# Optimization experiments

Hardware: AMD Instinct MI355X
Metric: run time of the kernel (lower is better)

## Reference

```python
import jax, jax.numpy as jnp
import numpy as np

TEMPERATURE = 0.07
EPS = 1e-12  # matches torch F.normalize default


def _l2_normalize(x):
    # torch F.normalize: x / max(||x||_2, eps)
    norm = jnp.sqrt(jnp.sum(x * x, axis=-1, keepdims=True))
    return x / jnp.maximum(norm, EPS)


def setup_inputs() -> dict:
    key = jax.random.key(0)
    k1, k2, k3 = jax.random.split(key, 3)
    B, N, D = 4096, 127, 256
    anchor = jax.random.normal(k1, (B, D), dtype=jnp.float32)
    positive = jax.random.normal(k2, (B, D), dtype=jnp.float32)
    negatives = jax.random.normal(k3, (B, N, D), dtype=jnp.float32)
    return {"anchor": anchor, "positive": positive, "negatives": negatives}


def reference(anchor, positive, negatives):
    a = _l2_normalize(anchor)          # [B, D]
    p = _l2_normalize(positive)        # [B, D]
    n = _l2_normalize(negatives)       # [B, N, D]
    pos_scores = jnp.sum(a * p, axis=-1, keepdims=True)   # [B, 1]
    neg_scores = jnp.einsum("bd,bnd->bn", a, n)           # [B, N]
    logits = jnp.concatenate([pos_scores, neg_scores], axis=1) / TEMPERATURE
    # cross-entropy with label 0 for every row
    loss = jnp.mean(jax.nn.logsumexp(logits, axis=-1) - logits[:, 0])
    return loss
```

## Files before the change

### kernel.cpp

```cpp
#include <hip/hip_runtime.h>
#include <math.h>


namespace {
constexpr int B = 4096;
constexpr int N = 127;
constexpr int D = 256;
constexpr int V = N + 1;
constexpr float INV_TEMP = 1.0f / 0.07f;
constexpr float EPS = 1e-12f;

typedef float f32x4 __attribute__((ext_vector_type(4)));

__device__ __forceinline__ float group16_reduce_sum(float v) {
    #pragma unroll
    for (int off = 1; off < 16; off <<= 1) v += __shfl_xor(v, off, 64);
    return v;
}
__device__ __forceinline__ float wave_reduce_sum(float v) {
    #pragma unroll
    for (int off = 32; off > 0; off >>= 1) v += __shfl_xor(v, off, 64);
    return v;
}
__device__ __forceinline__ float wave_reduce_max(float v) {
    #pragma unroll
    for (int off = 32; off > 0; off >>= 1) v = fmaxf(v, __shfl_xor(v, off, 64));
    return v;
}

__device__ __forceinline__ void load4(f32x4 (&buf)[4], const float* p) {
    #pragma unroll
    for (int i = 0; i < 4; ++i)
        buf[i] = *reinterpret_cast<const f32x4*>(p + i * 64);
}

__device__ __forceinline__ void acc4(float& d, float& s,
                                     const f32x4 (&aa)[4], const f32x4 (&x)[4]) {
    float dd = 0.f, ss = 0.f;
    #pragma unroll
    for (int i = 0; i < 4; ++i) {
        dd += aa[i].x * x[i].x + aa[i].y * x[i].y + aa[i].z * x[i].z + aa[i].w * x[i].w;
        ss += x[i].x * x[i].x + x[i].y * x[i].y + x[i].z * x[i].z + x[i].w * x[i].w;
    }
    d = dd; s = ss;
}
}

__global__ __launch_bounds__(256) void infonce_rows(
    const float* __restrict__ anchor,
    const float* __restrict__ positive,
    const float* __restrict__ negatives,
    float* __restrict__ row_loss)
{
    const int b   = blockIdx.x;
    const int tid = threadIdx.x;
    const int sub = tid & 15;
    const int g   = tid >> 4;

    __shared__ float scores[V];

    const float* arow = anchor + (size_t)b * D + sub * 4;
    f32x4 aa[4];
    load4(aa, arow);
    float asq = 0.f;
    #pragma unroll
    for (int i = 0; i < 4; ++i)
        asq += aa[i].x * aa[i].x + aa[i].y * aa[i].y + aa[i].z * aa[i].z + aa[i].w * aa[i].w;
    asq = group16_reduce_sum(asq);
    const float ainv = 1.0f / fmaxf(sqrtf(asq), EPS);
    #pragma unroll
    for (int i = 0; i < 4; ++i) aa[i] *= ainv;

    const float* nbase = negatives
        + ((ptrdiff_t)b * N + (ptrdiff_t)g - 1) * D + sub * 4;
    const float* p0 = (g == 0) ? (positive + (size_t)b * D + sub * 4) : nbase;

    float dot[8], sq[8];
    f32x4 bufA[4], bufB[4];
    load4(bufA, p0);
    #pragma unroll
    for (int itp = 0; itp < 4; ++itp) {
        const int it0 = 2 * itp, it1 = it0 + 1;
        load4(bufB, nbase + (size_t)it1 * 16 * D);
        acc4(dot[it0], sq[it0], aa, bufA);
        if (it1 + 1 < 8)
            load4(bufA, nbase + (size_t)(it1 + 1) * 16 * D);
        acc4(dot[it1], sq[it1], aa, bufB);
    }

    #pragma unroll
    for (int it = 0; it < 8; ++it) {
        const float d = group16_reduce_sum(dot[it]);
        const float s = group16_reduce_sum(sq[it]);
        if (sub == 0)
            scores[g + 16 * it] = d / fmaxf(sqrtf(s), EPS);
    }
    __syncthreads();

    if (tid < 64) {
        const float s0 = scores[tid]      * INV_TEMP;
        const float s1 = scores[tid + 64] * INV_TEMP;
        float m = wave_reduce_max(fmaxf(s0, s1));
        float e = expf(s0 - m) + expf(s1 - m);
        e = wave_reduce_sum(e);
        if (tid == 0)
            row_loss[b] = m + logf(e) - scores[0] * INV_TEMP;
    }
}

__global__ __launch_bounds__(256) void reduce_mean(
    const float* __restrict__ row_loss, float* __restrict__ out)
{
    __shared__ float wsum[4];
    const int tid  = threadIdx.x;
    const int wave = tid >> 6;
    const int lane = tid & 63;

    float s = 0.0f;
    for (int i = tid; i < B; i += 256) s += row_loss[i];
    s = wave_reduce_sum(s);
    if (lane == 0) wsum[wave] = s;
    __syncthreads();
    if (tid == 0)
        out[0] = (wsum[0] + wsum[1] + wsum[2] + wsum[3]) * (1.0f / (float)B);
}

extern "C" void kernel_launch(void* const* d_in, const int* in_sizes, int n_in,
                              void* d_out, int out_size, void* d_ws, size_t ws_size,
                              hipStream_t stream) {
    const float* anchor    = (const float*)d_in[0];
    const float* positive  = (const float*)d_in[1];
    const float* negatives = (const float*)d_in[2];
    float* out      = (float*)d_out;
    float* row_loss = (float*)d_ws;

    infonce_rows<<<B, 256, 0, stream>>>(anchor, positive, negatives, row_loss);
    reduce_mean<<<1, 256, 0, stream>>>(row_loss, out);
}
```

Measured before the change: 675.6 us.

## Assign one full row per wave with wave-wide reductions and register prefetch ring

Remaps the per-row dot-product work so each 64-lane wave handles a whole 256-element vector instead of 16-lane groups handling four chunks each. Loads rotate through a 4-deep register ring, and each row is reduced with full-wave shuffles. This aims to simplify addressing and reduce register use, but it increases shuffle reduction work per row and lowers the number of outstanding loads per thread.

```diff
diff --git a/kernel.cpp b/kernel.cpp
--- a/kernel.cpp
+++ b/kernel.cpp
@@ -12,11 +12,6 @@
 
 typedef float f32x4 __attribute__((ext_vector_type(4)));
 
-__device__ __forceinline__ float group16_reduce_sum(float v) {
-    #pragma unroll
-    for (int off = 1; off < 16; off <<= 1) v += __shfl_xor(v, off, 64);
-    return v;
-}
 __device__ __forceinline__ float wave_reduce_sum(float v) {
     #pragma unroll
     for (int off = 32; off > 0; off >>= 1) v += __shfl_xor(v, off, 64);
@@ -27,23 +22,6 @@
     for (int off = 32; off > 0; off >>= 1) v = fmaxf(v, __shfl_xor(v, off, 64));
     return v;
 }
-
-__device__ __forceinline__ void load4(f32x4 (&buf)[4], const float* p) {
-    #pragma unroll
-    for (int i = 0; i < 4; ++i)
-        buf[i] = *reinterpret_cast<const f32x4*>(p + i * 64);
-}
-
-__device__ __forceinline__ void acc4(float& d, float& s,
-                                     const f32x4 (&aa)[4], const f32x4 (&x)[4]) {
-    float dd = 0.f, ss = 0.f;
-    #pragma unroll
-    for (int i = 0; i < 4; ++i) {
-        dd += aa[i].x * x[i].x + aa[i].y * x[i].y + aa[i].z * x[i].z + aa[i].w * x[i].w;
-        ss += x[i].x * x[i].x + x[i].y * x[i].y + x[i].z * x[i].z + x[i].w * x[i].w;
-    }
-    d = dd; s = ss;
-}
 }
 
 __global__ __launch_bounds__(256) void infonce_rows(
@@ -52,48 +30,45 @@
     const float* __restrict__ negatives,
     float* __restrict__ row_loss)
 {
-    const int b   = blockIdx.x;
-    const int tid = threadIdx.x;
-    const int sub = tid & 15;
-    const int g   = tid >> 4;
+    const int b    = blockIdx.x;
+    const int tid  = threadIdx.x;
+    const int lane = tid & 63;
+    const int w    = tid >> 6;
 
     __shared__ float scores[V];
 
-    const float* arow = anchor + (size_t)b * D + sub * 4;
-    f32x4 aa[4];
-    load4(aa, arow);
-    float asq = 0.f;
+    f32x4 aa = *reinterpret_cast<const f32x4*>(anchor + (size_t)b * D + lane * 4);
+    float asq = aa.x * aa.x + aa.y * aa.y + aa.z * aa.z + aa.w * aa.w;
+    asq = wave_reduce_sum(asq);
+    const float ainv = 1.0f / fmaxf(sqrtf(asq), EPS);
+    aa *= ainv;
+
+    const float* nb = negatives
+        + ((ptrdiff_t)b * N + (ptrdiff_t)w - 1) * D + lane * 4;
+    const float* p0 = (w == 0) ? (positive + (size_t)b * D + lane * 4) : nb;
+
+    f32x4 buf[4];
+    buf[0] = *reinterpret_cast<const f32x4*>(p0);
     #pragma unroll
-    for (int i = 0; i < 4; ++i)
-        asq += aa[i].x * aa[i].x + aa[i].y * aa[i].y + aa[i].z * aa[i].z + aa[i].w * aa[i].w;
-    asq = group16_reduce_sum(asq);
-    const float ainv = 1.0f / fmaxf(sqrtf(asq), EPS);
-    #pragma unroll
-    for (int i = 0; i < 4; ++i) aa[i] *= ainv;
+    for (int j = 1; j < 4; ++j)
+        buf[j] = *reinterpret_cast<const f32x4*>(nb + (size_t)j * 4 * D);
 
-    const float* nbase = negatives
-        + ((ptrdiff_t)b * N + (ptrdiff_t)g - 1) * D + sub * 4;
-    const float* p0 = (g == 0) ? (positive + (size_t)b * D + sub * 4) : nbase;
-
-    float dot[8], sq[8];
-    f32x4 bufA[4], bufB[4];
-    load4(bufA, p0);
-    #pragma unroll
-    for (int itp = 0; itp < 4; ++itp) {
-        const int it0 = 2 * itp, it1 = it0 + 1;
-        load4(bufB, nbase + (size_t)it1 * 16 * D);
-        acc4(dot[it0], sq[it0], aa, bufA);
-        if (it1 + 1 < 8)
-            load4(bufA, nbase + (size_t)(it1 + 1) * 16 * D);
-        acc4(dot[it1], sq[it1], aa, bufB);
-    }
-
-    #pragma unroll
-    for (int it = 0; it < 8; ++it) {
-        const float d = group16_reduce_sum(dot[it]);
-        const float s = group16_reduce_sum(sq[it]);
-        if (sub == 0)
-            scores[g + 16 * it] = d / fmaxf(sqrtf(s), EPS);
+    const float* pn = nb + (size_t)16 * D;
+    for (int c = 0; c < 8; ++c) {
+        #pragma unroll
+        for (int j = 0; j < 4; ++j) {
+            const int it = 4 * c + j;
+            const f32x4 x = buf[j];
+            if (c < 7)
+                buf[j] = *reinterpret_cast<const f32x4*>(pn + (size_t)j * 4 * D);
+            float d = aa.x * x.x + aa.y * x.y + aa.z * x.z + aa.w * x.w;
+            float s = x.x * x.x + x.y * x.y + x.z * x.z + x.w * x.w;
+            d = wave_reduce_sum(d);
+            s = wave_reduce_sum(s);
+            if (lane == 0)
+                scores[w + 4 * it] = d / fmaxf(sqrtf(s), EPS);
+        }
+        pn += (size_t)16 * D;
     }
     __syncthreads();
 
```

Result: slower. 689.3 us (+2.0%).
